# Optimization experiments

Measured on AMD Instinct MI355X. Metric: run time of the kernel, lower is better.

## Reference

```python
import jax, jax.numpy as jnp
import numpy as np

B, L, D, H = 4, 1024, 768, 12
DH = D // H  # 64


def setup_inputs() -> dict:
    key = jax.random.key(0)
    kx, kk, kq, kv = jax.random.split(key, 4)
    # Original uses torch.rand (uniform [0,1)); scale by 1/D so pre-softmax
    # logits stay in a numerically sane range (same math, better conditioning).
    scale = 1.0 / D
    x = jax.random.normal(kx, (B, L, D), dtype=jnp.float32)
    k = jax.random.uniform(kk, (H, D, D), dtype=jnp.float32) * scale
    q = jax.random.uniform(kq, (H, D, D), dtype=jnp.float32) * scale
    v = jax.random.uniform(kv, (H, DH, D), dtype=jnp.float32) * scale
    return {"x": x, "k": k, "q": q, "v": v}


def reference(x, k, q, v):
    # x: [B, L, D]; torch permutes to [B, D, L] then 'bdl,ncd->bncl';
    # equivalent directly: 'bld,ncd->bncl'.
    K = jnp.einsum('bld,ncd->bncl', x, k)   # [B, H, D, L]
    Q = jnp.einsum('bld,ncd->bncl', x, q)   # [B, H, D, L]
    V = jnp.einsum('bld,ncd->bncl', x, v)   # [B, H, DH, L]
    scores = jnp.einsum('bndl,bndm->bnlm', Q, K)        # [B, H, L, L]
    S = jax.nn.softmax(scores, axis=-1)                  # softmax over dim 3
    R = jnp.einsum('bnkl,bndl->bndk', S, V)              # [B, H, DH, L]
    R = R.reshape(x.shape[0], D, -1)                     # [B, D, L]
    return jnp.transpose(R, (0, 2, 1))                   # [B, L, D]
```

## Files before the change

### kernel.cpp

```cpp
#include <hip/hip_runtime.h>
#include <hip/hip_bf16.h>
#include <stdint.h>
#include <stddef.h>

typedef unsigned short u16;
typedef __attribute__((ext_vector_type(8))) short short8;
typedef __attribute__((ext_vector_type(4))) float f32x4;
typedef __attribute__((ext_vector_type(16))) float f32x16;

#define NB 4
#define NL 1024
#define ND 768
#define NH 12
#define NDH 64

__device__ __forceinline__ u16 f2bf(float f) {
  __hip_bfloat16 h = __float2bfloat16(f);
  return *reinterpret_cast<u16*>(&h);
}
__device__ __forceinline__ float bf2f(u16 u) {
  __hip_bfloat16 h;
  *reinterpret_cast<u16*>(&h) = u;
  return __bfloat162float(h);
}

__device__ __forceinline__ void load16_to_lds(const u16* g, u16* l) {
  __builtin_amdgcn_global_load_lds(
      (__attribute__((address_space(1))) void*)(uintptr_t)g,
      (__attribute__((address_space(3))) void*)(uint32_t)(uintptr_t)l,
      16, 0, 0);
}

__global__ __launch_bounds__(256) void cast_bf16_kernel(const float* __restrict__ in,
                                                        u16* __restrict__ out, int n4) {
  int i = blockIdx.x * 256 + threadIdx.x;
  int stride = gridDim.x * 256;
  for (; i < n4; i += stride) {
    float4 f = ((const float4*)in)[i];
    ushort4 o;
    o.x = f2bf(f.x); o.y = f2bf(f.y); o.z = f2bf(f.z); o.w = f2bf(f.w);
    ((ushort4*)out)[i] = o;
  }
}

__global__ __launch_bounds__(256) void transpose_cast_kernel(const float* __restrict__ in,
                                                             u16* __restrict__ out) {
  __shared__ float tile[32][33];
  int h = blockIdx.z;
  const float* src = in + (size_t)h * ND * ND;
  u16* dst = out + (size_t)h * ND * ND;
  int c0 = blockIdx.x * 32, r0 = blockIdx.y * 32;
  int tx = threadIdx.x & 31, ty = threadIdx.x >> 5;
#pragma unroll
  for (int i = 0; i < 32; i += 8)
    tile[ty + i][tx] = src[(size_t)(r0 + ty + i) * ND + c0 + tx];
  __syncthreads();
#pragma unroll
  for (int i = 0; i < 32; i += 8)
    dst[(size_t)(c0 + ty + i) * ND + r0 + tx] = f2bf(tile[tx][ty + i]);
}

template <bool BF16_OUT, int IM, int IN, int KDIM, int LDC>
__global__ __launch_bounds__(256, 4) void gemm_bt(
    const u16* __restrict__ A, const u16* __restrict__ Bm, void* __restrict__ Cv,
    long sAb, long sAn, long sAz,
    long sBb, long sBn, long sBz,
    long sCb, long sCn, long sCz,
    int p0) {
  constexpr int BK = 64;
  constexpr int MTILE = IM * 64;
  constexpr int NTILE = IN * 64;
  constexpr int CPR = BK / 8;
  constexpr int ACH = MTILE * CPR / 256;
  constexpr int BCH = NTILE * CPR / 256;
  __shared__ __align__(16) u16 As[MTILE * BK];
  __shared__ __align__(16) u16 Bs[NTILE * BK];

  int id = blockIdx.x + gridDim.x * (blockIdx.y + gridDim.y * blockIdx.z);
  int total = gridDim.x * gridDim.y * gridDim.z;
  int xx, yy, zz;
  if ((total & 7) == 0) {
    int per = total >> 3;
    int wk = (id & 7) * per + (id >> 3);
    xx = wk % gridDim.x;
    int g2 = wk / gridDim.x;
    yy = g2 % gridDim.y;
    zz = g2 / gridDim.y;
  } else {
    xx = blockIdx.x; yy = blockIdx.y; zz = blockIdx.z;
  }

  int g = p0 + zz;
  int b = g / NH, n = g % NH;
  A  += (size_t)b * sAb + (size_t)n * sAn + (size_t)zz * sAz;
  Bm += (size_t)b * sBb + (size_t)n * sBn + (size_t)zz * sBz;
  size_t cOff = (size_t)b * sCb + (size_t)n * sCn + (size_t)zz * sCz;

  int m0 = yy * MTILE, n0 = xx * NTILE;
  int t = threadIdx.x;
  int lane = t & 63, w = t >> 6;
  int m32 = lane & 31, kg = lane >> 5;
  int wm = w >> 1, wn = w & 1;

  const u16* gAb;
  const u16* gBb;
  {
    int r = t / CPR;
    int cc = (t & (CPR - 1)) ^ (r & 7);
    gAb = A + (size_t)(m0 + r) * KDIM + cc * 8;
    gBb = Bm + (size_t)(n0 + r) * KDIM + cc * 8;
  }

  f32x16 acc[IM][IN];
#pragma unroll
  for (int i = 0; i < IM; i++)
#pragma unroll
    for (int j = 0; j < IN; j++)
#pragma unroll
      for (int r = 0; r < 16; r++) acc[i][j][r] = 0.f;

#pragma unroll 1
  for (int k0 = 0; k0 < KDIM; k0 += BK) {
    __syncthreads();
#pragma unroll
    for (int u = 0; u < ACH; u++)
      load16_to_lds(gAb + (size_t)u * 32 * KDIM, &As[(size_t)(u * 256 + w * 64) * 8]);
    gAb += BK;
#pragma unroll
    for (int u = 0; u < BCH; u++)
      load16_to_lds(gBb + (size_t)u * 32 * KDIM, &Bs[(size_t)(u * 256 + w * 64) * 8]);
    gBb += BK;
    __syncthreads();

#pragma unroll
    for (int kc = 0; kc < 2; kc++) {
      short8 af[IM][2], bfr[IN][2];
#pragma unroll
      for (int i = 0; i < IM; i++) {
        int row = wm * (IM * 32) + i * 32 + m32;
#pragma unroll
        for (int h = 0; h < 2; h++) {
          int ck = (kc * 4 + h * 2 + kg) ^ (row & 7);
          af[i][h] = *(const short8*)&As[row * BK + ck * 8];
        }
      }
#pragma unroll
      for (int j = 0; j < IN; j++) {
        int row = wn * (IN * 32) + j * 32 + m32;
#pragma unroll
        for (int h = 0; h < 2; h++) {
          int ck = (kc * 4 + h * 2 + kg) ^ (row & 7);
          bfr[j][h] = *(const short8*)&Bs[row * BK + ck * 8];
        }
      }
#pragma unroll
      for (int i = 0; i < IM; i++)
#pragma unroll
        for (int j = 0; j < IN; j++) {
          acc[i][j] = __builtin_amdgcn_mfma_f32_32x32x16_bf16(af[i][0], bfr[j][0], acc[i][j], 0, 0, 0);
          acc[i][j] = __builtin_amdgcn_mfma_f32_32x32x16_bf16(af[i][1], bfr[j][1], acc[i][j], 0, 0, 0);
        }
    }
  }

#pragma unroll
  for (int i = 0; i < IM; i++) {
#pragma unroll
    for (int j = 0; j < IN; j++) {
      int colg = n0 + wn * (IN * 32) + j * 32 + m32;
#pragma unroll
      for (int r = 0; r < 16; r++) {
        int rowg = m0 + wm * (IM * 32) + i * 32 + (r & 3) + 8 * (r >> 2) + 4 * kg;
        float vv = acc[i][j][r];
        if (BF16_OUT) {
          ((u16*)Cv)[cOff + (size_t)rowg * LDC + colg] = f2bf(vv);
        } else {
          ((float*)Cv)[cOff + (size_t)rowg * LDC + colg] = vv;
        }
      }
    }
  }
}

__global__ __launch_bounds__(256) void softmax_pv_kernel(
    const u16* __restrict__ Sb, const u16* __restrict__ V2, float* __restrict__ out,
    int p0) {
  __shared__ __align__(16) u16 Ps[64 * 128];
  __shared__ __align__(16) u16 Vs[64 * 128];

  int id = blockIdx.x + gridDim.x * blockIdx.y;
  int total = gridDim.x * gridDim.y;
  int xx, zz;
  if ((total & 7) == 0) {
    int per = total >> 3;
    int wk = (id & 7) * per + (id >> 3);
    xx = wk & 15; zz = wk >> 4;
  } else {
    xx = blockIdx.x; zz = blockIdx.y;
  }

  int g = p0 + zz;
  int b = g / NH, n = g % NH;
  const u16* S = Sb + (size_t)zz * NL * NL;
  const u16* V = V2 + (size_t)zz * NDH * NL;

  int l0 = xx * 64;
  int t = threadIdx.x;
  int lane = t & 63, w = t >> 6;
  int row16 = lane & 15, q = lane >> 4;
  int rs = row16 & 7;

  f32x4 acc[5];
#pragma unroll
  for (int j = 0; j < 5; j++) acc[j] = (f32x4){0.f, 0.f, 0.f, 0.f};

  short8 onesf;
  {
    short val = (row16 == 0) ? (short)0x3F80 : (short)0;
#pragma unroll
    for (int e = 0; e < 8; e++) onesf[e] = val;
  }

  const u16* ssrc[4];
  const u16* vsrc[4];
#pragma unroll
  for (int u = 0; u < 4; u++) {
    int c = u * 256 + t;
    int r = c >> 4, cc = (c & 15) ^ (r & 7);
    ssrc[u] = S + (size_t)(l0 + r) * NL + cc * 8;
    vsrc[u] = V + (size_t)r * NL + cc * 8;
  }

#pragma unroll 1
  for (int mt = 0; mt < 8; mt++) {
    int mo = mt * 128;
    __syncthreads();
#pragma unroll
    for (int u = 0; u < 4; u++)
      load16_to_lds(ssrc[u] + mo, &Ps[(size_t)(u * 256 + w * 64) * 8]);
#pragma unroll
    for (int u = 0; u < 4; u++)
      load16_to_lds(vsrc[u] + mo, &Vs[(size_t)(u * 256 + w * 64) * 8]);
    __syncthreads();

#pragma unroll
    for (int kk = 0; kk < 4; kk++) {
      int ch = ((kk * 4 + q) ^ rs) * 16;
      int lrow = w * 16 + row16;
      short8 raw = *(const short8*)((const char*)Ps + lrow * 256 + ch);
      short8 af;
#pragma unroll
      for (int e = 0; e < 8; e++) af[e] = (short)f2bf(__expf(bf2f((u16)raw[e])));
      short8 bfr[4];
#pragma unroll
      for (int j = 0; j < 4; j++) {
        int dh = j * 16 + row16;
        bfr[j] = *(const short8*)((const char*)Vs + dh * 256 + ch);
      }
#pragma unroll
      for (int j = 0; j < 4; j++)
        acc[j] = __builtin_amdgcn_mfma_f32_16x16x32_bf16(af, bfr[j], acc[j], 0, 0, 0);
      acc[4] = __builtin_amdgcn_mfma_f32_16x16x32_bf16(af, onesf, acc[4], 0, 0, 0);
    }
  }

#pragma unroll
  for (int r = 0; r < 4; r++) {
    float sum = __shfl(acc[4][r], lane & 48, 64);
    float inv = 1.0f / sum;
    int row = l0 + w * 16 + q * 4 + r;
    float* op = out + ((size_t)b * NL + row) * ND + n * NDH;
#pragma unroll
    for (int j = 0; j < 4; j++)
      op[j * 16 + row16] = acc[j][r] * inv;
  }
}

extern "C" void kernel_launch(void* const* d_in, const int* in_sizes, int n_in,
                              void* d_out, int out_size, void* d_ws, size_t ws_size,
                              hipStream_t stream) {
  (void)in_sizes; (void)n_in; (void)out_size;
  const float* x  = (const float*)d_in[0];
  const float* kI = (const float*)d_in[1];
  const float* qI = (const float*)d_in[2];
  const float* vI = (const float*)d_in[3];
  float* out = (float*)d_out;

  size_t off = 0;
  char* wsb = (char*)d_ws;
  auto alloc = [&](size_t bytes) -> char* {
    char* p = wsb + off;
    off += (bytes + 255) & ~(size_t)255;
    return p;
  };
  u16* xb = (u16*)alloc((size_t)NB * NL * ND * 2);
  u16* qT = (u16*)alloc((size_t)NH * ND * ND * 2);
  u16* kT = (u16*)alloc((size_t)NH * ND * ND * 2);
  u16* vb = (u16*)alloc((size_t)NH * NDH * ND * 2);
  u16* MT = (u16*)alloc((size_t)NH * ND * ND * 2);
  size_t fixedSz = off;
  const size_t perPair = (size_t)NL * ND * 2 + (size_t)NL * NL * 2 + (size_t)NDH * NL * 2;
  int chunk = NB * NH;
  if (fixedSz + (size_t)chunk * perPair > ws_size) {
    size_t avail = ws_size > fixedSz ? ws_size - fixedSz : 0;
    chunk = (int)(avail / perPair);
    if (chunk < 1) chunk = 1;
    if (chunk > NB * NH) chunk = NB * NH;
  }
  u16* T  = (u16*)alloc((size_t)chunk * NL * ND * 2);
  u16* Sb = (u16*)alloc((size_t)chunk * NL * NL * 2);
  u16* V2 = (u16*)alloc((size_t)chunk * NDH * NL * 2);

  const long DD  = (long)ND * ND;
  const long LD  = (long)NL * ND;
  const long LL  = (long)NL * NL;
  const long DHD = (long)NDH * ND;
  const long DHL = (long)NDH * NL;

  {
    int n4 = NB * NL * ND / 4;
    cast_bf16_kernel<<<dim3((n4 + 255) / 256), dim3(256), 0, stream>>>(x, xb, n4);
    int n4v = NH * NDH * ND / 4;
    cast_bf16_kernel<<<dim3((n4v + 255) / 256), dim3(256), 0, stream>>>(vI, vb, n4v);
  }
  transpose_cast_kernel<<<dim3(24, 24, NH), dim3(256), 0, stream>>>(qI, qT);
  transpose_cast_kernel<<<dim3(24, 24, NH), dim3(256), 0, stream>>>(kI, kT);

  gemm_bt<true, 2, 2, 768, ND><<<dim3(6, 6, NH), dim3(256), 0, stream>>>(
      kT, qT, MT,
      0, DD, 0,  0, DD, 0,  0, DD, 0, 0);

  for (int p0 = 0; p0 < NB * NH; p0 += chunk) {
    int c = NB * NH - p0;
    if (c > chunk) c = chunk;
    gemm_bt<true, 1, 1, 768, NL><<<dim3(16, 1, c), dim3(256), 0, stream>>>(
        vb, xb, V2,
        0, DHD, 0,  LD, 0, 0,  0, 0, DHL, p0);
    gemm_bt<true, 2, 2, 768, ND><<<dim3(6, 8, c), dim3(256), 0, stream>>>(
        xb, MT, T,
        LD, 0, 0,  0, DD, 0,  0, 0, LD, p0);
    gemm_bt<true, 2, 2, 768, NL><<<dim3(8, 8, c), dim3(256), 0, stream>>>(
        T, xb, Sb,
        0, 0, LD,  LD, 0, 0,  0, 0, LL, p0);
    softmax_pv_kernel<<<dim3(16, c), dim3(256), 0, stream>>>(Sb, V2, out, p0);
  }
}
```

Baseline: 310.8 us.

## Load V fragments directly from global in softmax-PV and reorder GEMM fragment loads

The softmax-PV kernel no longer stages V tiles through shared memory. Each lane reads its V fragments straight from global memory (expected to hit cache) and LDS use is halved, with launch bounds raised to request higher occupancy. The GEMM inner loop now loads A/B fragments per k-half instead of both halves at once, which lowers register pressure. The trade-off is more global load latency in the PV loop and less load-ahead in the GEMM.

```diff
diff --git a/kernel.cpp b/kernel.cpp
--- a/kernel.cpp
+++ b/kernel.cpp
@@ -134,32 +134,27 @@
 
 #pragma unroll
     for (int kc = 0; kc < 2; kc++) {
-      short8 af[IM][2], bfr[IN][2];
-#pragma unroll
-      for (int i = 0; i < IM; i++) {
-        int row = wm * (IM * 32) + i * 32 + m32;
-#pragma unroll
-        for (int h = 0; h < 2; h++) {
+#pragma unroll
+      for (int h = 0; h < 2; h++) {
+        short8 af[IM], bfr[IN];
+#pragma unroll
+        for (int i = 0; i < IM; i++) {
+          int row = wm * (IM * 32) + i * 32 + m32;
           int ck = (kc * 4 + h * 2 + kg) ^ (row & 7);
-          af[i][h] = *(const short8*)&As[row * BK + ck * 8];
+          af[i] = *(const short8*)&As[row * BK + ck * 8];
         }
+#pragma unroll
+        for (int j = 0; j < IN; j++) {
+          int row = wn * (IN * 32) + j * 32 + m32;
+          int ck = (kc * 4 + h * 2 + kg) ^ (row & 7);
+          bfr[j] = *(const short8*)&Bs[row * BK + ck * 8];
+        }
+#pragma unroll
+        for (int i = 0; i < IM; i++)
+#pragma unroll
+          for (int j = 0; j < IN; j++)
+            acc[i][j] = __builtin_amdgcn_mfma_f32_32x32x16_bf16(af[i], bfr[j], acc[i][j], 0, 0, 0);
       }
-#pragma unroll
-      for (int j = 0; j < IN; j++) {
-        int row = wn * (IN * 32) + j * 32 + m32;
-#pragma unroll
-        for (int h = 0; h < 2; h++) {
-          int ck = (kc * 4 + h * 2 + kg) ^ (row & 7);
-          bfr[j][h] = *(const short8*)&Bs[row * BK + ck * 8];
-        }
-      }
-#pragma unroll
-      for (int i = 0; i < IM; i++)
-#pragma unroll
-        for (int j = 0; j < IN; j++) {
-          acc[i][j] = __builtin_amdgcn_mfma_f32_32x32x16_bf16(af[i][0], bfr[j][0], acc[i][j], 0, 0, 0);
-          acc[i][j] = __builtin_amdgcn_mfma_f32_32x32x16_bf16(af[i][1], bfr[j][1], acc[i][j], 0, 0, 0);
-        }
     }
   }
 
@@ -182,11 +177,10 @@
   }
 }
 
-__global__ __launch_bounds__(256) void softmax_pv_kernel(
+__global__ __launch_bounds__(256, 6) void softmax_pv_kernel(
     const u16* __restrict__ Sb, const u16* __restrict__ V2, float* __restrict__ out,
     int p0) {
   __shared__ __align__(16) u16 Ps[64 * 128];
-  __shared__ __align__(16) u16 Vs[64 * 128];
 
   int id = blockIdx.x + gridDim.x * blockIdx.y;
   int total = gridDim.x * gridDim.y;
@@ -222,14 +216,16 @@
   }
 
   const u16* ssrc[4];
-  const u16* vsrc[4];
 #pragma unroll
   for (int u = 0; u < 4; u++) {
     int c = u * 256 + t;
     int r = c >> 4, cc = (c & 15) ^ (r & 7);
     ssrc[u] = S + (size_t)(l0 + r) * NL + cc * 8;
-    vsrc[u] = V + (size_t)r * NL + cc * 8;
-  }
+  }
+  const u16* vp[4];
+#pragma unroll
+  for (int j = 0; j < 4; j++)
+    vp[j] = V + (size_t)(j * 16 + row16) * NL + q * 8;
 
 #pragma unroll 1
   for (int mt = 0; mt < 8; mt++) {
@@ -238,25 +234,20 @@
 #pragma unroll
     for (int u = 0; u < 4; u++)
       load16_to_lds(ssrc[u] + mo, &Ps[(size_t)(u * 256 + w * 64) * 8]);
-#pragma unroll
-    for (int u = 0; u < 4; u++)
-      load16_to_lds(vsrc[u] + mo, &Vs[(size_t)(u * 256 + w * 64) * 8]);
     __syncthreads();
 
 #pragma unroll
     for (int kk = 0; kk < 4; kk++) {
+      short8 bfr[4];
+#pragma unroll
+      for (int j = 0; j < 4; j++)
+        bfr[j] = *(const short8*)(vp[j] + mo + kk * 32);
       int ch = ((kk * 4 + q) ^ rs) * 16;
       int lrow = w * 16 + row16;
       short8 raw = *(const short8*)((const char*)Ps + lrow * 256 + ch);
       short8 af;
 #pragma unroll
       for (int e = 0; e < 8; e++) af[e] = (short)f2bf(__expf(bf2f((u16)raw[e])));
-      short8 bfr[4];
-#pragma unroll
-      for (int j = 0; j < 4; j++) {
-        int dh = j * 16 + row16;
-        bfr[j] = *(const short8*)((const char*)Vs + dh * 256 + ch);
-      }
 #pragma unroll
       for (int j = 0; j < 4; j++)
         acc[j] = __builtin_amdgcn_mfma_f32_16x16x32_bf16(af, bfr[j], acc[j], 0, 0, 0);
```

Measured after the change: 352.9 us. 13.5% more time.
